# Performance work log

Measured on AMD Instinct MI355X. Metric: run time of the kernel, lower is better.

The kernel has to match this reference:

```python
import jax, jax.numpy as jnp
import numpy as np

BS, C, H, W = 16, 64, 128, 128
NC = 80          # num classes (hardcoded 80 in original via expand(-1, 80, -1))
TOPK = 128
TAU = 0.07
EPS = 1e-12      # F.normalize eps


def setup_inputs() -> dict:
    key = jax.random.key(0)
    k1, k2, k3, k4 = jax.random.split(key, 4)
    feat = jax.random.normal(k1, (BS, C, H, W), dtype=jnp.float32)
    score = jax.random.uniform(k2, (BS, NC, H, W), dtype=jnp.float32)
    # hm: GT heatmap with exactly one 1.0 peak per (batch, class) for ~half the classes
    pos = jax.random.randint(k3, (BS, NC), 0, H * W)
    present = jax.random.bernoulli(k4, 0.5, (BS, NC)).astype(jnp.float32)
    b = jnp.arange(BS)[:, None]
    c = jnp.arange(NC)[None, :]
    hm = jnp.zeros((BS, NC, H * W), jnp.float32).at[b, c, pos].set(present)
    hm = hm.reshape(BS, NC, H, W)
    return {"feat": feat, "score": score, "hm": hm}


def reference(feat, score, hm):
    bs, c, h, w = feat.shape
    nc = hm.shape[1]
    hw = h * w
    score = jax.lax.stop_gradient(score)  # score.detach()

    # F.normalize(feat, dim=1)
    feat = feat / jnp.maximum(jnp.linalg.norm(feat, axis=1, keepdims=True), EPS)

    # q: feature at the hm==1 peak of each present class (one peak per (b,cls))
    peak = (hm == 1.0).astype(feat.dtype)                       # [bs,nc,h,w]
    q = jnp.einsum('bnhw,bchw->bnc', peak, feat)                # [bs,nc,c]
    class_mask = (peak.sum(axis=(2, 3)) > 0).astype(feat.dtype)  # [bs,nc]

    # k0: hm-weighted pooled feature per class, L2-normalized
    k0 = jnp.einsum('bchw,bnhw->bnc', feat, hm)                 # [bs,nc,c]
    k0 = k0 / jnp.maximum(jnp.linalg.norm(k0, axis=-1, keepdims=True), EPS)

    # mask score: zero at GT locations and for absent classes
    hm_free = (hm.sum(axis=1) == 0).astype(score.dtype)         # [bs,h,w]
    score = score * hm_free[:, None] * class_mask[:, :, None, None]

    max_values = score.max(axis=1).reshape(bs, hw)              # [bs,hw]
    class_indices = score.argmax(axis=1).reshape(bs, hw)        # [bs,hw]
    topk_values, topk_indices = jax.lax.top_k(max_values, TOPK)  # [bs,topk]
    k_all_mask_t = (topk_values > 0).astype(feat.dtype)         # [bs,topk]
    topk_class = jnp.take_along_axis(class_indices, topk_indices, axis=1)  # [bs,topk]

    feat_flat = feat.reshape(bs, c, hw)
    k_top = jnp.take_along_axis(feat_flat, topk_indices[:, None, :], axis=2)  # [bs,c,topk]
    k_top = k_top.transpose(0, 2, 1)                            # [bs,topk,c]

    # pseudo heatmap: 0.9 at selected (class, pos) pairs with positive score
    b_idx = jnp.arange(bs)[:, None]
    pseudo_hm = jnp.zeros((bs, nc, hw), feat.dtype).at[
        b_idx, topk_class, topk_indices].set(k_all_mask_t * 0.9)
    pseudo_hm = pseudo_hm.reshape(bs, nc, h, w)

    # positive mask: selected positions whose pseudo class matches the query class
    class_ids = jnp.arange(nc, dtype=feat.dtype)
    target = jnp.where(class_mask[:, :, None] == 1, class_ids[None, :, None], -1.0)  # [bs,nc,1]
    k_mask_top = (target == topk_class[:, None, :].astype(feat.dtype)).astype(feat.dtype)
    k_mask_top = k_mask_top * k_all_mask_t[:, None, :]          # [bs,nc,topk]
    k0_mask = class_mask[:, :, None] * jnp.eye(nc, dtype=feat.dtype)  # [bs,nc,nc]

    k_all = jnp.concatenate([k_top, k0], axis=1)                # [bs,topk+nc,c]
    k_mask = jnp.concatenate([k_mask_top, k0_mask], axis=-1)    # [bs,nc,topk+nc]
    k_all_mask = jnp.concatenate([k_all_mask_t, class_mask], axis=-1)  # [bs,topk+nc]

    sim = jnp.exp(jnp.einsum('bnc,bkc->bnk', q, k_all) / TAU)   # [bs,nc,topk+nc]
    sim_sum = (sim * k_all_mask[:, None, :]).sum(-1, keepdims=True)
    sim_sum = jnp.where(sim_sum == 0, 1.0, sim_sum)
    logit = jnp.where(k_mask > 0, sim / sim_sum, 1.0)
    log_loss = (jnp.log(logit) * k_mask).sum(-1)                # [bs,nc]
    num = k_mask.sum(-1)
    num = jnp.where(num == 0, 1.0, num)
    count = class_mask.sum()
    loss = ((log_loss / num) * class_mask).sum() / count
    return (-loss, pseudo_hm)
```

## Files before the change

kernel.cpp:

```cpp
#include <hip/hip_runtime.h>
#include <math.h>

#define BS 16
#define C 64
#define H 128
#define W 128
#define HW (H*W)
#define NC 80
#define TOPK 128
#define KALL (TOPK+NC)
#define TAU 0.07f
#define EPSN 1e-12f

__global__ void k_init(int* peak_pos, int* has_peak) {
    int stride = gridDim.x * blockDim.x;
    int tid = blockIdx.x * blockDim.x + threadIdx.x;
    for (int i = tid; i < BS * HW; i += stride) has_peak[i] = 0;
    for (int i = tid; i < BS * NC; i += stride) peak_pos[i] = -1;
}

__global__ void k_peak(const float* __restrict__ hm, int* peak_pos, int* has_peak) {
    int bn = blockIdx.x;
    int b = bn / NC;
    const float* p = hm + (size_t)bn * HW;
    for (int i = threadIdx.x; i < HW; i += blockDim.x) {
        if (p[i] == 1.0f) {
            peak_pos[bn] = i;
            has_peak[b * HW + i] = 1;
        }
    }
}

__global__ void k_max(const float* __restrict__ score, const int* __restrict__ peak_pos,
                      const int* __restrict__ has_peak,
                      float* __restrict__ maxv, int* __restrict__ clsidx) {
    __shared__ float cm[NC];
    int b = blockIdx.y;
    int p = blockIdx.x * blockDim.x + threadIdx.x;
    if (threadIdx.x < NC)
        cm[threadIdx.x] = (peak_pos[b * NC + threadIdx.x] >= 0) ? 1.0f : 0.0f;
    __syncthreads();
    float hf = has_peak[b * HW + p] ? 0.0f : 1.0f;
    const float* sb = score + (size_t)b * NC * HW + p;
    float best = sb[0] * cm[0] * hf;
    int bi = 0;
    for (int n = 1; n < NC; ++n) {
        float v = sb[(size_t)n * HW] * cm[n] * hf;
        if (v > best) { best = v; bi = n; }
    }
    maxv[b * HW + p] = best;
    clsidx[b * HW + p] = bi;
}

__global__ __launch_bounds__(1024) void k_topk(const float* __restrict__ maxv,
                                               const int* __restrict__ clsidx,
                                               float* __restrict__ topkv,
                                               int* __restrict__ topki,
                                               int* __restrict__ topkc) {
    __shared__ unsigned int hist[2048];
    __shared__ unsigned int wtot[16];
    __shared__ unsigned int woff[16];
    __shared__ unsigned int s_pref;
    __shared__ int s_rank;
    __shared__ unsigned int s_bin;
    __shared__ unsigned int s_above;

    int b = blockIdx.x, t = threadIdx.x;
    int lane = t & 63, wid = t >> 6;
    unsigned int key[16];
    const float* mv = maxv + (size_t)b * HW;
    #pragma unroll
    for (int j = 0; j < 16; ++j) key[j] = __float_as_uint(mv[t * 16 + j]);

    if (t == 0) { s_pref = 0u; s_rank = TOPK; }

    const int shifts[3] = {21, 10, 0};
    const int widths[3] = {11, 11, 10};

    for (int rnd = 0; rnd < 3; ++rnd) {
        int sh = shifts[rnd], w = widths[rnd];
        unsigned mask = (1u << w) - 1u;
        hist[t] = 0u; hist[t + 1024] = 0u;
        __syncthreads();
        unsigned pref = s_pref;
        int hiShift = sh + w;
        #pragma unroll
        for (int j = 0; j < 16; ++j) {
            unsigned k = key[j];
            bool ok = (rnd == 0) || ((k >> hiShift) == pref);
            if (ok) atomicAdd(&hist[(k >> sh) & mask], 1u);
        }
        __syncthreads();
        unsigned p = hist[2 * t] + hist[2 * t + 1];
        unsigned s = p;
        #pragma unroll
        for (int off = 1; off < 64; off <<= 1) {
            unsigned o = __shfl_down(s, off);
            if (lane + off < 64) s += o;
        }
        if (lane == 0) wtot[wid] = s;
        __syncthreads();
        if (wid == 0) {
            unsigned vv = (lane < 16) ? wtot[lane] : 0u;
            unsigned ss = vv;
            #pragma unroll
            for (int off = 1; off < 64; off <<= 1) {
                unsigned o = __shfl_down(ss, off);
                if (lane + off < 64) ss += o;
            }
            if (lane < 16) woff[lane] = ss - vv;
        }
        __syncthreads();
        unsigned S_t = s + woff[wid];
        unsigned S_next = S_t - p;
        int r = s_rank;
        if ((int)S_t >= r && (int)S_next < r) {
            unsigned hi = hist[2 * t + 1];
            if ((int)(S_next + hi) >= r) { s_bin = 2u * t + 1u; s_above = S_next; }
            else                         { s_bin = 2u * t;      s_above = S_next + hi; }
        }
        __syncthreads();
        if (t == 0) {
            s_pref = (s_pref << w) | s_bin;
            s_rank = s_rank - (int)s_above;
        }
        __syncthreads();
    }
    unsigned K = s_pref;
    int need_eq = s_rank;
    int cnt_gt = TOPK - need_eq;

    int cg = 0, ce = 0;
    #pragma unroll
    for (int j = 0; j < 16; ++j) { cg += (key[j] > K); ce += (key[j] == K); }
    unsigned v = ((unsigned)cg << 16) | (unsigned)ce;
    unsigned sc = v;
    #pragma unroll
    for (int off = 1; off < 64; off <<= 1) {
        unsigned o = __shfl_up(sc, off);
        if (lane >= off) sc += o;
    }
    if (lane == 63) wtot[wid] = sc;
    __syncthreads();
    if (wid == 0) {
        unsigned vv = (lane < 16) ? wtot[lane] : 0u;
        unsigned ss = vv;
        #pragma unroll
        for (int off = 1; off < 64; off <<= 1) {
            unsigned o = __shfl_up(ss, off);
            if (lane >= off) ss += o;
        }
        if (lane < 16) woff[lane] = ss - vv;
    }
    __syncthreads();
    unsigned ex = (sc - v) + woff[wid];
    int pg = (int)(ex >> 16);
    int pe = (int)(ex & 0xffffu);
    int lg = 0, le = 0;
    #pragma unroll
    for (int j = 0; j < 16; ++j) {
        unsigned k = key[j];
        int slot = -1;
        if (k > K) { slot = pg + lg; ++lg; }
        else if (k == K) { int er = pe + le; ++le; if (er < need_eq) slot = cnt_gt + er; }
        if (slot >= 0) {
            int idx = t * 16 + j;
            topkv[b * TOPK + slot] = __uint_as_float(k);
            topki[b * TOPK + slot] = idx;
            topkc[b * TOPK + slot] = clsidx[(size_t)b * HW + idx];
        }
    }
}

__global__ void k_gather(const float* __restrict__ feat, const int* __restrict__ peak_pos,
                         const int* __restrict__ topki, float* k_all, float* qv) {
    int bk = blockIdx.x;
    int b = bk / KALL, k = bk % KALL, c = threadIdx.x;
    int pos;
    if (k < TOPK) {
        pos = topki[b * TOPK + k];
    } else {
        int n = k - TOPK;
        int pp = peak_pos[b * NC + n];
        if (pp < 0) {
            k_all[((size_t)b * KALL + k) * C + c] = 0.0f;
            qv[((size_t)b * NC + n) * C + c] = 0.0f;
            return;
        }
        pos = pp;
    }
    float v = feat[((size_t)b * C + c) * HW + pos];
    float ss = v * v;
    #pragma unroll
    for (int off = 1; off < 64; off <<= 1) ss += __shfl_xor(ss, off);
    float qc = v / fmaxf(sqrtf(ss), EPSN);
    if (k < TOPK) {
        k_all[((size_t)b * KALL + k) * C + c] = qc;
    } else {
        int n = k - TOPK;
        qv[((size_t)b * NC + n) * C + c] = qc;
        float qq = qc * qc;
        #pragma unroll
        for (int off = 1; off < 64; off <<= 1) qq += __shfl_xor(qq, off);
        k_all[((size_t)b * KALL + k) * C + c] = qc / fmaxf(sqrtf(qq), EPSN);
    }
}

__global__ void k_loss(const float* __restrict__ k_all, const float* __restrict__ qv,
                       const int* __restrict__ peak_pos, const float* __restrict__ topkv,
                       const int* __restrict__ topkc, float* loss_bn) {
    __shared__ float qs[C];
    __shared__ float r1[256];
    __shared__ float r2[256];
    __shared__ float s_simsum, s_num;
    int bn = blockIdx.x;
    int b = bn / NC, n = bn % NC, t = threadIdx.x;
    if (peak_pos[bn] < 0) { if (t == 0) loss_bn[bn] = 0.0f; return; }
    if (t < C) qs[t] = qv[(size_t)bn * C + t];
    __syncthreads();
    float sim = 0.0f, kam = 0.0f, km = 0.0f;
    if (t < KALL) {
        const float* kr = k_all + ((size_t)b * KALL + t) * C;
        float dot = 0.0f;
        for (int c2 = 0; c2 < C; ++c2) dot += qs[c2] * kr[c2];
        sim = expf(dot / TAU);
        if (t < TOPK) {
            float posm = (topkv[b * TOPK + t] > 0.0f) ? 1.0f : 0.0f;
            kam = posm;
            km = (topkc[b * TOPK + t] == n) ? posm : 0.0f;
        } else {
            int j = t - TOPK;
            kam = (peak_pos[b * NC + j] >= 0) ? 1.0f : 0.0f;
            km = (j == n) ? 1.0f : 0.0f;
        }
    }
    r1[t] = sim * kam;
    r2[t] = km;
    __syncthreads();
    for (int s = 128; s > 0; s >>= 1) {
        if (t < s) { r1[t] += r1[t + s]; r2[t] += r2[t + s]; }
        __syncthreads();
    }
    if (t == 0) {
        float ss = r1[0];
        s_simsum = (ss == 0.0f) ? 1.0f : ss;
        s_num = (r2[0] == 0.0f) ? 1.0f : r2[0];
    }
    __syncthreads();
    r1[t] = (km > 0.0f) ? logf(sim / s_simsum) : 0.0f;
    __syncthreads();
    for (int s = 128; s > 0; s >>= 1) {
        if (t < s) r1[t] += r1[t + s];
        __syncthreads();
    }
    if (t == 0) loss_bn[bn] = r1[0] / s_num;
}

__global__ void k_scatter(const float* __restrict__ topkv, const int* __restrict__ topki,
                          const int* __restrict__ topkc, float* out) {
    int i = blockIdx.x * blockDim.x + threadIdx.x;
    if (i >= BS * TOPK) return;
    int b = i / TOPK;
    if (topkv[i] > 0.0f)
        out[1 + ((size_t)b * NC + topkc[i]) * HW + topki[i]] = 0.9f;
}

__global__ void k_final(const float* __restrict__ loss_bn, const int* __restrict__ peak_pos,
                        float* out) {
    __shared__ float r1[256];
    __shared__ float r2[256];
    int t = threadIdx.x;
    float s = 0.0f, cnt = 0.0f;
    for (int i = t; i < BS * NC; i += 256) {
        s += loss_bn[i];
        cnt += (peak_pos[i] >= 0) ? 1.0f : 0.0f;
    }
    r1[t] = s; r2[t] = cnt;
    __syncthreads();
    for (int st = 128; st > 0; st >>= 1) {
        if (t < st) { r1[t] += r1[t + st]; r2[t] += r2[t + st]; }
        __syncthreads();
    }
    if (t == 0) out[0] = -(r1[0] / r2[0]);
}

extern "C" void kernel_launch(void* const* d_in, const int* in_sizes, int n_in,
                              void* d_out, int out_size, void* d_ws, size_t ws_size,
                              hipStream_t stream) {
    const float* feat  = (const float*)d_in[0];
    const float* score = (const float*)d_in[1];
    const float* hm    = (const float*)d_in[2];
    float* out = (float*)d_out;

    char* ws = (char*)d_ws;
    size_t off = 0;
    auto alloc = [&](size_t bytes) -> void* {
        void* p = ws + off;
        off += (bytes + 255) & ~(size_t)255;
        return p;
    };
    int*   peak_pos = (int*)  alloc((size_t)BS * NC * 4);
    int*   has_peak = (int*)  alloc((size_t)BS * HW * 4);
    float* maxv     = (float*)alloc((size_t)BS * HW * 4);
    int*   clsidx   = (int*)  alloc((size_t)BS * HW * 4);
    float* topkv    = (float*)alloc((size_t)BS * TOPK * 4);
    int*   topki    = (int*)  alloc((size_t)BS * TOPK * 4);
    int*   topkc    = (int*)  alloc((size_t)BS * TOPK * 4);
    float* k_all    = (float*)alloc((size_t)BS * KALL * C * 4);
    float* qv       = (float*)alloc((size_t)BS * NC * C * 4);
    float* loss_bn  = (float*)alloc((size_t)BS * NC * 4);

    hipMemsetAsync(d_out, 0, (size_t)out_size * sizeof(float), stream);
    k_init<<<512, 256, 0, stream>>>(peak_pos, has_peak);
    k_peak<<<BS * NC, 256, 0, stream>>>(hm, peak_pos, has_peak);
    dim3 gmax(HW / 256, BS);
    k_max<<<gmax, 256, 0, stream>>>(score, peak_pos, has_peak, maxv, clsidx);
    k_topk<<<BS, 1024, 0, stream>>>(maxv, clsidx, topkv, topki, topkc);
    k_gather<<<BS * KALL, 64, 0, stream>>>(feat, peak_pos, topki, k_all, qv);
    k_loss<<<BS * NC, 256, 0, stream>>>(k_all, qv, peak_pos, topkv, topkc, loss_bn);
    k_scatter<<<(BS * TOPK + 255) / 256, 256, 0, stream>>>(topkv, topki, topkc, out);
    k_final<<<1, 256, 0, stream>>>(loss_bn, peak_pos, out);
}
```

Before: 116.4 us.

## Drop has_peak map and init kernel; vectorize peak, max and topk loads

Removes the k_init kernel and the per-pixel has_peak buffer. k_max now checks GT peak positions against the 80 per-class peak positions held in shared memory. k_peak becomes a float4 scan with a wave and block max-reduction that writes peak_pos directly, which also sets -1 for absent classes. k_max processes four pixels per thread with float4 loads and int4 stores, and k_topk loads its keys as float4. The aim is to cut one launch, a 1 MB init and read, and scattered memory traffic, at the cost of 80 compares per pixel in registers and fewer threads in k_max.

```diff
diff --git a/kernel.cpp b/kernel.cpp
--- a/kernel.cpp
+++ b/kernel.cpp
@@ -12,44 +12,68 @@
 #define TAU 0.07f
 #define EPSN 1e-12f
 
-__global__ void k_init(int* peak_pos, int* has_peak) {
-    int stride = gridDim.x * blockDim.x;
-    int tid = blockIdx.x * blockDim.x + threadIdx.x;
-    for (int i = tid; i < BS * HW; i += stride) has_peak[i] = 0;
-    for (int i = tid; i < BS * NC; i += stride) peak_pos[i] = -1;
-}
-
-__global__ void k_peak(const float* __restrict__ hm, int* peak_pos, int* has_peak) {
-    int bn = blockIdx.x;
-    int b = bn / NC;
-    const float* p = hm + (size_t)bn * HW;
-    for (int i = threadIdx.x; i < HW; i += blockDim.x) {
-        if (p[i] == 1.0f) {
-            peak_pos[bn] = i;
-            has_peak[b * HW + i] = 1;
-        }
+__global__ __launch_bounds__(1024) void k_peak(const float* __restrict__ hm,
+                                               int* __restrict__ peak_pos) {
+    __shared__ int wmax[16];
+    int bn = blockIdx.x, t = threadIdx.x;
+    int lane = t & 63, wid = t >> 6;
+    const float4* p = (const float4*)(hm + (size_t)bn * HW);
+    int found = -1;
+    #pragma unroll
+    for (int j = 0; j < 4; ++j) {
+        int gi = j * 1024 + t;
+        float4 v = p[gi];
+        int base = gi * 4;
+        if (v.x == 1.0f) found = base;
+        if (v.y == 1.0f) found = base + 1;
+        if (v.z == 1.0f) found = base + 2;
+        if (v.w == 1.0f) found = base + 3;
+    }
+    #pragma unroll
+    for (int off = 1; off < 64; off <<= 1) found = max(found, __shfl_xor(found, off));
+    if (lane == 0) wmax[wid] = found;
+    __syncthreads();
+    if (t == 0) {
+        int m = wmax[0];
+        #pragma unroll
+        for (int i = 1; i < 16; ++i) m = max(m, wmax[i]);
+        peak_pos[bn] = m;
     }
 }
 
 __global__ void k_max(const float* __restrict__ score, const int* __restrict__ peak_pos,
-                      const int* __restrict__ has_peak,
                       float* __restrict__ maxv, int* __restrict__ clsidx) {
-    __shared__ float cm[NC];
+    __shared__ int pk[NC];
     int b = blockIdx.y;
-    int p = blockIdx.x * blockDim.x + threadIdx.x;
-    if (threadIdx.x < NC)
-        cm[threadIdx.x] = (peak_pos[b * NC + threadIdx.x] >= 0) ? 1.0f : 0.0f;
-    __syncthreads();
-    float hf = has_peak[b * HW + p] ? 0.0f : 1.0f;
-    const float* sb = score + (size_t)b * NC * HW + p;
-    float best = sb[0] * cm[0] * hf;
-    int bi = 0;
+    int g = blockIdx.x * blockDim.x + threadIdx.x;
+    if (threadIdx.x < NC) pk[threadIdx.x] = peak_pos[b * NC + threadIdx.x];
+    __syncthreads();
+    const float4* sb = (const float4*)(score + (size_t)b * NC * HW);
+    int p0 = g * 4;
+    int pp0 = pk[0];
+    float m0 = (pp0 >= 0) ? 1.0f : 0.0f;
+    float4 v0 = sb[g];
+    float bx = v0.x * m0, by = v0.y * m0, bz = v0.z * m0, bw = v0.w * m0;
+    int ix = 0, iy = 0, iz = 0, iw = 0;
+    bool pe0 = (pp0 == p0), pe1 = (pp0 == p0 + 1), pe2 = (pp0 == p0 + 2), pe3 = (pp0 == p0 + 3);
+    #pragma unroll 8
     for (int n = 1; n < NC; ++n) {
-        float v = sb[(size_t)n * HW] * cm[n] * hf;
-        if (v > best) { best = v; bi = n; }
-    }
-    maxv[b * HW + p] = best;
-    clsidx[b * HW + p] = bi;
+        int pp = pk[n];
+        float m = (pp >= 0) ? 1.0f : 0.0f;
+        float4 v = sb[(size_t)n * (HW / 4) + g];
+        float vx = v.x * m, vy = v.y * m, vz = v.z * m, vw = v.w * m;
+        if (vx > bx) { bx = vx; ix = n; }
+        if (vy > by) { by = vy; iy = n; }
+        if (vz > bz) { bz = vz; iz = n; }
+        if (vw > bw) { bw = vw; iw = n; }
+        pe0 |= (pp == p0); pe1 |= (pp == p0 + 1); pe2 |= (pp == p0 + 2); pe3 |= (pp == p0 + 3);
+    }
+    if (pe0) { bx = 0.0f; ix = 0; }
+    if (pe1) { by = 0.0f; iy = 0; }
+    if (pe2) { bz = 0.0f; iz = 0; }
+    if (pe3) { bw = 0.0f; iw = 0; }
+    ((float4*)maxv)[(size_t)b * (HW / 4) + g] = make_float4(bx, by, bz, bw);
+    ((int4*)clsidx)[(size_t)b * (HW / 4) + g] = make_int4(ix, iy, iz, iw);
 }
 
 __global__ __launch_bounds__(1024) void k_topk(const float* __restrict__ maxv,
@@ -68,9 +92,15 @@
     int b = blockIdx.x, t = threadIdx.x;
     int lane = t & 63, wid = t >> 6;
     unsigned int key[16];
-    const float* mv = maxv + (size_t)b * HW;
-    #pragma unroll
-    for (int j = 0; j < 16; ++j) key[j] = __float_as_uint(mv[t * 16 + j]);
+    const float4* mv4 = (const float4*)(maxv + (size_t)b * HW);
+    #pragma unroll
+    for (int j4 = 0; j4 < 4; ++j4) {
+        float4 v = mv4[t * 4 + j4];
+        key[j4 * 4 + 0] = __float_as_uint(v.x);
+        key[j4 * 4 + 1] = __float_as_uint(v.y);
+        key[j4 * 4 + 2] = __float_as_uint(v.z);
+        key[j4 * 4 + 3] = __float_as_uint(v.w);
+    }
 
     if (t == 0) { s_pref = 0u; s_rank = TOPK; }
 
@@ -300,7 +330,6 @@
         return p;
     };
     int*   peak_pos = (int*)  alloc((size_t)BS * NC * 4);
-    int*   has_peak = (int*)  alloc((size_t)BS * HW * 4);
     float* maxv     = (float*)alloc((size_t)BS * HW * 4);
     int*   clsidx   = (int*)  alloc((size_t)BS * HW * 4);
     float* topkv    = (float*)alloc((size_t)BS * TOPK * 4);
@@ -311,10 +340,9 @@
     float* loss_bn  = (float*)alloc((size_t)BS * NC * 4);
 
     hipMemsetAsync(d_out, 0, (size_t)out_size * sizeof(float), stream);
-    k_init<<<512, 256, 0, stream>>>(peak_pos, has_peak);
-    k_peak<<<BS * NC, 256, 0, stream>>>(hm, peak_pos, has_peak);
-    dim3 gmax(HW / 256, BS);
-    k_max<<<gmax, 256, 0, stream>>>(score, peak_pos, has_peak, maxv, clsidx);
+    k_peak<<<BS * NC, 1024, 0, stream>>>(hm, peak_pos);
+    dim3 gmax(HW / 4 / 256, BS);
+    k_max<<<gmax, 256, 0, stream>>>(score, peak_pos, maxv, clsidx);
     k_topk<<<BS, 1024, 0, stream>>>(maxv, clsidx, topkv, topki, topkc);
     k_gather<<<BS * KALL, 64, 0, stream>>>(feat, peak_pos, topki, k_all, qv);
     k_loss<<<BS * NC, 256, 0, stream>>>(k_all, qv, peak_pos, topkv, topkc, loss_bn);
```

Result: faster. 100.3 us (-13.8%).
